# Optimization experiments

Hardware: AMD Instinct MI355X
Metric: run time of the kernel (lower is better)

Reference implementation:

```python
import jax, jax.numpy as jnp
import numpy as np


def setup_inputs() -> dict:
    key = jax.random.key(0)
    k_x, k_q, k_k, k_v = jax.random.split(key, 4)
    B, S, E, D = 4, 2048, 1024, 1024
    scale = 1.0 / np.sqrt(E)
    return {
        "x": jax.random.normal(k_x, (B, S, E), dtype=jnp.float32),
        # nn.Linear weight matrices, shape [out_dim, in_dim]; y = x @ W.T
        "w_q": jax.random.normal(k_q, (D, E), dtype=jnp.float32) * scale,
        "w_k": jax.random.normal(k_k, (D, E), dtype=jnp.float32) * scale,
        "w_v": jax.random.normal(k_v, (D, E), dtype=jnp.float32) * scale,
    }


def reference(x, w_q, w_k, w_v):
    # x: [B, S, E]; w_*: [D, E] (torch nn.Linear convention)
    B, S, E = x.shape
    q = jnp.einsum("bse,de->bsd", x, w_q)  # [B, S, D]
    k = jnp.einsum("bse,de->bsd", x, w_k)
    v = jnp.einsum("bse,de->bsd", x, w_v)
    D = q.shape[-1]
    # raw scores, then causal mask (strictly upper triangle -> -inf), then
    # scale by 1/sqrt(D) inside softmax exactly as the original does.
    scores = jnp.einsum("bsd,btd->bst", q, k)  # [B, S, S]
    causal = jnp.tril(jnp.ones((S, S), dtype=bool))  # True = keep
    scores = jnp.where(causal[None], scores, -jnp.inf)
    attn = jax.nn.softmax(scores / jnp.sqrt(jnp.asarray(D, x.dtype)), axis=-1)
    # dropout p=0.0 -> identity
    return jnp.einsum("bst,btd->bsd", attn, v)  # [B, S, D]
```

## Files before the change

kernel.cpp:

```cpp
#include <hip/hip_runtime.h>
#include <hip/hip_bf16.h>


typedef unsigned short u16;
typedef __attribute__((ext_vector_type(4))) u16   u16x4;
typedef __attribute__((ext_vector_type(8))) u16   u16x8;
typedef __attribute__((ext_vector_type(8))) short short8;
typedef __attribute__((ext_vector_type(4))) float f32x4;
typedef __attribute__((ext_vector_type(4))) int   i32x4;

__device__ inline u16 f2b(float v) {
    __hip_bfloat16 b = __float2bfloat16(v);
    return *reinterpret_cast<u16*>(&b);
}
__device__ inline float b2f(u16 v) {
    unsigned int u = ((unsigned int)v) << 16;
    return *reinterpret_cast<float*>(&u);
}

template <typename T> __device__ inline void store_elem(T* p, float v);
template <> __device__ inline void store_elem<float>(float* p, float v) { *p = v; }
template <> __device__ inline void store_elem<u16>(u16* p, float v)     { *p = f2b(v); }

__device__ inline void gload_lds16(const u16* g, u16* l) {
    __builtin_amdgcn_global_load_lds(
        (const __attribute__((address_space(1))) void*)g,
        (__attribute__((address_space(3))) void*)l, 16, 0, 0);
}

__global__ __launch_bounds__(256) void cast_all_kernel(
    const float* __restrict__ x,  const float* __restrict__ wq,
    const float* __restrict__ wk, const float* __restrict__ wv,
    u16* __restrict__ dst) {
    int q = blockIdx.x * 256 + threadIdx.x;
    const float* src;
    int sidx;
    if (q < 2097152) { src = x; sidx = q * 4; }
    else {
        int qq = q - 2097152;
        int w  = qq >> 18;
        sidx   = (qq & 262143) * 4;
        src    = (w == 0) ? wq : (w == 1) ? wk : wv;
    }
    float4 v = *(const float4*)(src + sidx);
    u16x4 o;
    o.x = f2b(v.x); o.y = f2b(v.y); o.z = f2b(v.z); o.w = f2b(v.w);
    *(u16x4*)(dst + q * 4) = o;
}

__global__ __launch_bounds__(512) void gemm_qkv256(
    const u16* __restrict__ xb, const u16* __restrict__ wb,
    u16* __restrict__ qk, u16* __restrict__ vt)
{
    __shared__ __align__(16) u16 lds[2][2][16384];

    const int tid  = threadIdx.x;
    const int lane = tid & 63;
    const int wave = tid >> 6;
    const int quad = lane >> 4;
    const int r16  = lane & 15;
    const int wm   = wave >> 2;
    const int wn   = wave & 3;

    int flat = blockIdx.x;
    int swz  = (flat & 7) * 48 + (flat >> 3);
    int bx   = swz % 12;
    int m0   = (swz / 12) * 256;
    const bool isV = (bx >= 8);
    const int  n0  = (isV ? bx - 8 : bx) * 256;
    const u16* __restrict__ Ab = xb;
    const u16* __restrict__ Bb = wb + (isV ? 2048 * 1024 : 0);

    int gA[2][2], gB[2][2], lA[2][2], lB[2][2];
    {
        const int cswz = ((lane & 3) * 8) ^ (((lane >> 5) & 1) << 4);
        const int rsub = lane >> 2;
#pragma unroll
        for (int u = 0; u < 2; ++u)
#pragma unroll
            for (int j = 0; j < 2; ++j) {
                int s   = j * 8 + wave;
                int sh  = s >> 1, cg = s & 1;
                int rgA = (sh & 3) + (sh >> 2) * 8 + u * 4;
                int rgB = sh + u * 8;
                int cl  = cg * 32 + cswz;
                gA[u][j] = (m0 + rgA * 16 + rsub) * 1024 + cl;
                gB[u][j] = (n0 + rgB * 16 + rsub) * 1024 + cl;
                lA[u][j] = (rgA * 2 + cg) * 512 + lane * 8;
                lB[u][j] = (rgB * 2 + cg) * 512 + lane * 8;
            }
    }

#define STAGE_A(BUF, U, KK) do { \
        gload_lds16(Ab + gA[U][0] + (KK), &lds[BUF][0][lA[U][0]]); \
        gload_lds16(Ab + gA[U][1] + (KK), &lds[BUF][0][lA[U][1]]); } while (0)
#define STAGE_B(BUF, U, KK) do { \
        gload_lds16(Bb + gB[U][0] + (KK), &lds[BUF][1][lB[U][0]]); \
        gload_lds16(Bb + gB[U][1] + (KK), &lds[BUF][1][lB[U][1]]); } while (0)

    const int cswr = (quad * 8) ^ ((r16 >> 3) << 4);
    const int rdA0 = wm * 16 * 512 + r16 * 32 + cswr;
    const int rdB0 = wn * 8  * 512 + r16 * 32 + cswr;

    f32x4 acc[8][4] = {};

    STAGE_B(0, 0, 0);  STAGE_B(0, 1, 0);  STAGE_A(0, 0, 0);  STAGE_A(0, 1, 0);
    STAGE_B(1, 0, 64); STAGE_B(1, 1, 64); STAGE_A(1, 0, 64); STAGE_A(1, 1, 64);
    asm volatile("s_waitcnt vmcnt(8)" ::: "memory");
    __builtin_amdgcn_s_barrier();

    for (int t = 0; t < 16; ++t) {
        const int  buf = t & 1;
        const int  kk2 = t * 64 + 128;
        const bool pf  = (t < 14);
        const u16* Al  = lds[buf][0];
        const u16* Bl  = lds[buf][1];
        short8 bfr[4][2], a01[2][2], a23[2][2], a45[2][2], a67[2][2];

#pragma unroll
        for (int nf = 0; nf < 4; ++nf)
#pragma unroll
            for (int ks = 0; ks < 2; ++ks)
                bfr[nf][ks] = *(const short8*)&Bl[rdB0 + (nf * 2 + ks) * 512];
#pragma unroll
        for (int mf = 0; mf < 2; ++mf)
#pragma unroll
            for (int ks = 0; ks < 2; ++ks)
                a01[mf][ks] = *(const short8*)&Al[rdA0 + (mf * 2 + ks) * 512];
        __builtin_amdgcn_s_barrier();
        __builtin_amdgcn_s_setprio(1);
#pragma unroll
        for (int mf = 0; mf < 2; ++mf)
#pragma unroll
            for (int nf = 0; nf < 4; ++nf)
#pragma unroll
                for (int ks = 0; ks < 2; ++ks)
                    acc[mf][nf] = __builtin_amdgcn_mfma_f32_16x16x32_bf16(
                        a01[mf][ks], bfr[nf][ks], acc[mf][nf], 0, 0, 0);
        __builtin_amdgcn_s_setprio(0);
        __builtin_amdgcn_s_barrier();

#pragma unroll
        for (int mf = 0; mf < 2; ++mf)
#pragma unroll
            for (int ks = 0; ks < 2; ++ks)
                a23[mf][ks] = *(const short8*)&Al[rdA0 + ((mf + 2) * 2 + ks) * 512];
        if (pf) STAGE_B(buf, 0, kk2);
        __builtin_amdgcn_s_barrier();
        __builtin_amdgcn_s_setprio(1);
#pragma unroll
        for (int mf = 0; mf < 2; ++mf)
#pragma unroll
            for (int nf = 0; nf < 4; ++nf)
#pragma unroll
                for (int ks = 0; ks < 2; ++ks)
                    acc[mf + 2][nf] = __builtin_amdgcn_mfma_f32_16x16x32_bf16(
                        a23[mf][ks], bfr[nf][ks], acc[mf + 2][nf], 0, 0, 0);
        __builtin_amdgcn_s_setprio(0);
        __builtin_amdgcn_s_barrier();

#pragma unroll
        for (int mf = 0; mf < 2; ++mf)
#pragma unroll
            for (int ks = 0; ks < 2; ++ks) {
                a45[mf][ks] = *(const short8*)&Al[rdA0 + ((mf + 4) * 2 + ks) * 512];
                a67[mf][ks] = *(const short8*)&Al[rdA0 + ((mf + 6) * 2 + ks) * 512];
            }
        if (pf) STAGE_B(buf, 1, kk2);
        __builtin_amdgcn_s_barrier();
        __builtin_amdgcn_s_setprio(1);
#pragma unroll
        for (int mf = 0; mf < 2; ++mf)
#pragma unroll
            for (int nf = 0; nf < 4; ++nf)
#pragma unroll
                for (int ks = 0; ks < 2; ++ks)
                    acc[mf + 4][nf] = __builtin_amdgcn_mfma_f32_16x16x32_bf16(
                        a45[mf][ks], bfr[nf][ks], acc[mf + 4][nf], 0, 0, 0);
        __builtin_amdgcn_s_setprio(0);
        asm volatile("s_waitcnt lgkmcnt(0)" ::: "memory");
        __builtin_amdgcn_s_barrier();

        if (pf) { STAGE_A(buf, 0, kk2); STAGE_A(buf, 1, kk2); }
        __builtin_amdgcn_s_barrier();
        __builtin_amdgcn_s_setprio(1);
#pragma unroll
        for (int mf = 0; mf < 2; ++mf)
#pragma unroll
            for (int nf = 0; nf < 4; ++nf)
#pragma unroll
                for (int ks = 0; ks < 2; ++ks)
                    acc[mf + 6][nf] = __builtin_amdgcn_mfma_f32_16x16x32_bf16(
                        a67[mf][ks], bfr[nf][ks], acc[mf + 6][nf], 0, 0, 0);
        __builtin_amdgcn_s_setprio(0);
        if (pf) asm volatile("s_waitcnt vmcnt(8)" ::: "memory");
        else    asm volatile("s_waitcnt vmcnt(0)" ::: "memory");
        __builtin_amdgcn_s_barrier();
    }
#undef STAGE_A
#undef STAGE_B

    if (!isV) {
#pragma unroll
        for (int mf = 0; mf < 8; ++mf) {
            int m = m0 + wm * 128 + mf * 16 + quad * 4;
#pragma unroll
            for (int nf = 0; nf < 4; ++nf) {
                int n = n0 + wn * 64 + nf * 16 + r16;
#pragma unroll
                for (int r = 0; r < 4; ++r)
                    qk[(m + r) * 2048 + n] = f2b(acc[mf][nf][r]);
            }
        }
    } else {
#pragma unroll
        for (int mf = 0; mf < 8; ++mf) {
            int mbase = m0 + wm * 128 + mf * 16 + quad * 4;
            int b = mbase >> 11;
            int s = mbase & 2047;
#pragma unroll
            for (int nf = 0; nf < 4; ++nf) {
                int d = n0 + wn * 64 + nf * 16 + r16;
                u16x4 o;
#pragma unroll
                for (int r = 0; r < 4; ++r) o[r] = f2b(acc[mf][nf][r]);
                *(u16x4*)(vt + (((b << 10) + d) * 2048 + s)) = o;
            }
        }
    }
}

#define MT 128
#define NT 128
#define BKH 32
#define HSZ (MT * BKH)

template <int TRANS, typename OutT>
__device__ __forceinline__ void gemm_core(
    u16* __restrict__ As, u16* __restrict__ Bs,
    const u16* __restrict__ Ab, int lda,
    const u16* __restrict__ Bb, int ldb,
    OutT* __restrict__ Cb, int ldc,
    int m0, int n0, int kbeg, int kend)
{
    const int tid  = threadIdx.x;
    const int lane = tid & 63;
    const int wave = tid >> 6;
    const int quad = lane >> 4;
    const int r16  = lane & 15;
    const int mw   = (wave >> 1) * 64;
    const int nw   = (wave & 1) * 64;

    const int c0 = tid, c1 = tid + 256;
    const int r0 = c0 >> 2, k0 = (c0 & 3) * 8;
    const int r1 = c1 >> 2, k1 = (c1 & 3) * 8;
    const int oa0 = (m0 + r0) * lda + k0;
    const int oa1 = (m0 + r1) * lda + k1;
    const int ob0 = (n0 + r0) * ldb + k0;
    const int ob1 = (n0 + r1) * ldb + k1;

    f32x4 acc[4][4] = {};

    for (int kk = kbeg; kk < kend; kk += 2 * BKH) {
        __syncthreads();
        gload_lds16(Ab + (kk + oa0),        &As[c0 * 8]);
        gload_lds16(Ab + (kk + oa1),        &As[c1 * 8]);
        gload_lds16(Ab + (kk + BKH + oa0),  &As[HSZ + c0 * 8]);
        gload_lds16(Ab + (kk + BKH + oa1),  &As[HSZ + c1 * 8]);
        gload_lds16(Bb + (kk + ob0),        &Bs[c0 * 8]);
        gload_lds16(Bb + (kk + ob1),        &Bs[c1 * 8]);
        gload_lds16(Bb + (kk + BKH + ob0),  &Bs[HSZ + c0 * 8]);
        gload_lds16(Bb + (kk + BKH + ob1),  &Bs[HSZ + c1 * 8]);
        __syncthreads();

#pragma unroll
        for (int h = 0; h < 2; h++) {
            short8 af[4], bf[4];
#pragma unroll
            for (int i = 0; i < 4; i++)
                af[i] = *(const short8*)&As[h * HSZ + (mw + i * 16 + r16) * BKH + quad * 8];
#pragma unroll
            for (int j = 0; j < 4; j++)
                bf[j] = *(const short8*)&Bs[h * HSZ + (nw + j * 16 + r16) * BKH + quad * 8];
#pragma unroll
            for (int i = 0; i < 4; i++)
#pragma unroll
                for (int j = 0; j < 4; j++)
                    acc[i][j] = __builtin_amdgcn_mfma_f32_16x16x32_bf16(af[i], bf[j], acc[i][j], 0, 0, 0);
        }
    }

    if (TRANS == 0) {
#pragma unroll
        for (int i = 0; i < 4; i++)
#pragma unroll
            for (int j = 0; j < 4; j++)
#pragma unroll
                for (int r = 0; r < 4; r++) {
                    int m = m0 + mw + i * 16 + quad * 4 + r;
                    int n = n0 + nw + j * 16 + r16;
                    store_elem(&Cb[(long long)m * ldc + n], acc[i][j][r]);
                }
    } else {
#pragma unroll
        for (int i = 0; i < 4; i++)
#pragma unroll
            for (int j = 0; j < 4; j++) {
                int mbase = m0 + mw + i * 16 + quad * 4;
                int d     = n0 + nw + j * 16 + r16;
                int b     = mbase >> 11;
                int s     = mbase & 2047;
                u16x4 o;
#pragma unroll
                for (int r = 0; r < 4; r++) o[r] = f2b(acc[i][j][r]);
                *(u16x4*)((u16*)Cb + (((b << 10) + d) * 2048 + s)) = o;
            }
    }
}

__global__ __launch_bounds__(256, 4) void gemm_scores(
    const u16* __restrict__ qk, u16* __restrict__ sc) {
    __shared__ __align__(16) u16 As[2 * HSZ];
    __shared__ __align__(16) u16 Bs[2 * HSZ];
    int t = blockIdx.x;
    float ff = sqrtf(8.0f * t + 1.0f);
    int m = (int)((ff - 1.0f) * 0.5f);
    while ((m + 1) * (m + 2) / 2 <= t) m++;
    while (m * (m + 1) / 2 > t) m--;
    int m0 = m * MT;
    int n0 = (t - m * (m + 1) / 2) * NT;
    const u16* Ab = qk + (long long)blockIdx.z * 2048 * 2048;
    const u16* Bb = Ab + 1024;
    u16* Cb = sc + (long long)blockIdx.z * 2048 * 2048;
    gemm_core<0, u16>(As, Bs, Ab, 2048, Bb, 2048, Cb, 2048, m0, n0, 0, 1024);
}

__global__ __launch_bounds__(256, 4) void gemm_pv(
    const u16* __restrict__ P, const u16* __restrict__ vt,
    float* __restrict__ out, float* __restrict__ part)
{
    __shared__ __align__(16) u16 As[2 * HSZ];
    __shared__ __align__(16) u16 Bs[2 * HSZ];
    const int bid = blockIdx.x;
    int m, chunk, n;
    if (bid < 80) {
        int q = bid >> 3; n = bid & 7;
        if (q < 9) { m = 7 + q; chunk = 0; } else { m = 15; chunk = 1; }
    } else {
        int r = bid - 80; int s = 7 - (r >> 4); int t = r & 15;
        n = t & 7;
        if (t < 8) { m = s - 1; chunk = 0; } else { m = s + 7; chunk = 1; }
    }
    const int m0 = m * MT, n0 = n * NT;
    const int kbeg = chunk ? 1024 : 0;
    const int kend = chunk ? (m0 + MT) : min(1024, m0 + MT);
    const int b = blockIdx.z;

    const u16* Ab = P  + (long long)b * 2048 * 2048;
    const u16* Bb = vt + (long long)b * 1024 * 2048;
    float* Cb = (chunk == 0)
        ? out  + (long long)b * 2097152
        : part + (long long)b * 1048576 - 1024LL * 1024;
    gemm_core<0, float>(As, Bs, Ab, 2048, Bb, 2048, Cb, 1024, m0, n0, kbeg, kend);
}

__global__ __launch_bounds__(256) void pv_combine(float* __restrict__ out,
                                                  const float* __restrict__ part) {
    long long idx = ((long long)blockIdx.x * 256 + threadIdx.x) * 8;
    long long bb = idx >> 20;
    long long j  = idx & 1048575;
    float* o = out + bb * 2097152 + 1048576 + j;
    const float* p = part + bb * 1048576 + j;
    float4 o0 = *(float4*)o, o1 = *(float4*)(o + 4);
    float4 p0 = *(const float4*)p, p1 = *(const float4*)(p + 4);
    o0.x += p0.x; o0.y += p0.y; o0.z += p0.z; o0.w += p0.w;
    o1.x += p1.x; o1.y += p1.y; o1.z += p1.z; o1.w += p1.w;
    *(float4*)o = o0; *(float4*)(o + 4) = o1;
}

__global__ __launch_bounds__(256) void softmax_kernel(const u16* __restrict__ sc,
                                                      u16* __restrict__ P) {
    const int S = 2048;
    int row = blockIdx.x;
    int i   = row & (S - 1);
    int n   = i + 1;
    int kendr = (i & ~127) + 128;
    const u16* srow = sc + (long long)row * S;
    u16*       prow = P  + (long long)row * S;

    int j0 = threadIdx.x * 8;
    u16x8 raw = {};
    if (j0 <= i) raw = *(const u16x8*)(srow + j0);
    float v[8];
#pragma unroll
    for (int e = 0; e < 8; e++) v[e] = (j0 + e < n) ? b2f(raw[e]) : -1e30f;

    __shared__ float red[8];
    float lmax = v[0];
#pragma unroll
    for (int e = 1; e < 8; e++) lmax = fmaxf(lmax, v[e]);
    for (int o = 32; o > 0; o >>= 1) lmax = fmaxf(lmax, __shfl_xor(lmax, o, 64));
    int wid = threadIdx.x >> 6;
    if ((threadIdx.x & 63) == 0) red[wid] = lmax;
    __syncthreads();
    float Mx = fmaxf(fmaxf(red[0], red[1]), fmaxf(red[2], red[3]));

    const float C = 0.045112384f;
    float ev[8];
    float lsum = 0.f;
#pragma unroll
    for (int e = 0; e < 8; e++) {
        ev[e] = (j0 + e < n) ? exp2f((v[e] - Mx) * C) : 0.f;
        lsum += ev[e];
    }
    for (int o = 32; o > 0; o >>= 1) lsum += __shfl_xor(lsum, o, 64);
    if ((threadIdx.x & 63) == 0) red[4 + wid] = lsum;
    __syncthreads();
    float inv = 1.0f / (red[4] + red[5] + red[6] + red[7]);

    if (j0 < kendr) {
        u16x8 o8;
#pragma unroll
        for (int e = 0; e < 8; e++) o8[e] = f2b(ev[e] * inv);
        *(u16x8*)(prow + j0) = o8;
    }
}

extern "C" void kernel_launch(void* const* d_in, const int* in_sizes, int n_in,
                              void* d_out, int out_size, void* d_ws, size_t ws_size,
                              hipStream_t stream) {
    const float* x  = (const float*)d_in[0];
    const float* wq = (const float*)d_in[1];
    const float* wk = (const float*)d_in[2];
    const float* wv = (const float*)d_in[3];
    float* out = (float*)d_out;

    char* ws = (char*)d_ws;
    u16*   xb   = (u16*)(ws);
    u16*   wb   = (u16*)(ws + 16777216LL);
    u16*   qk   = (u16*)(ws + 23068672LL);
    u16*   sc   = (u16*)(ws + 56623104LL);
    u16*   P    = (u16*)(ws + 90177536LL);
    u16*   vt   = (u16*)(ws + 123731968LL);
    float* part = (float*)(ws + 140509184LL);

    cast_all_kernel<<<11264, 256, 0, stream>>>(x, wq, wk, wv, xb);

    gemm_qkv256<<<384, 512, 0, stream>>>(xb, wb, qk, vt);

    gemm_scores<<<dim3(136, 1, 4), 256, 0, stream>>>(qk, sc);

    softmax_kernel<<<8192, 256, 0, stream>>>(sc, P);

    gemm_pv<<<dim3(192, 1, 4), 256, 0, stream>>>(P, vt, out, part);
    pv_combine<<<2048, 256, 0, stream>>>(out, part);
}
```

Measured before the change: 256.4 us.

## Move V projection into causal scores kernel and pair softmax rows per block

The V projection is taken out of the large QKV GEMM and computed by extra blocks appended to the triangular scores GEMM launch. Those extra blocks fill the load imbalance of the causal tiles, and the QK GEMM becomes a smaller launch. Softmax now handles a long row and a short row in each block, which evens out per-block work and halves the block count. The trade-off is that V now uses the smaller 128-tile GEMM core instead of the tuned 256-tile kernel, which may be less efficient for that part.

```diff
diff --git a/kernel.cpp b/kernel.cpp
--- a/kernel.cpp
+++ b/kernel.cpp
@@ -48,9 +48,9 @@
     *(u16x4*)(dst + q * 4) = o;
 }
 
-__global__ __launch_bounds__(512) void gemm_qkv256(
+__global__ __launch_bounds__(512) void gemm_qk256(
     const u16* __restrict__ xb, const u16* __restrict__ wb,
-    u16* __restrict__ qk, u16* __restrict__ vt)
+    u16* __restrict__ qk)
 {
     __shared__ __align__(16) u16 lds[2][2][16384];
 
@@ -63,13 +63,11 @@
     const int wn   = wave & 3;
 
     int flat = blockIdx.x;
-    int swz  = (flat & 7) * 48 + (flat >> 3);
-    int bx   = swz % 12;
-    int m0   = (swz / 12) * 256;
-    const bool isV = (bx >= 8);
-    const int  n0  = (isV ? bx - 8 : bx) * 256;
+    int swz  = (flat & 7) * 32 + (flat >> 3);
+    int m0   = (swz >> 3) * 256;
+    const int n0 = (swz & 7) * 256;
     const u16* __restrict__ Ab = xb;
-    const u16* __restrict__ Bb = wb + (isV ? 2048 * 1024 : 0);
+    const u16* __restrict__ Bb = wb;
 
     int gA[2][2], gB[2][2], lA[2][2], lB[2][2];
     {
@@ -200,32 +198,15 @@
 #undef STAGE_A
 #undef STAGE_B
 
-    if (!isV) {
-#pragma unroll
-        for (int mf = 0; mf < 8; ++mf) {
-            int m = m0 + wm * 128 + mf * 16 + quad * 4;
-#pragma unroll
-            for (int nf = 0; nf < 4; ++nf) {
-                int n = n0 + wn * 64 + nf * 16 + r16;
-#pragma unroll
-                for (int r = 0; r < 4; ++r)
-                    qk[(m + r) * 2048 + n] = f2b(acc[mf][nf][r]);
-            }
-        }
-    } else {
-#pragma unroll
-        for (int mf = 0; mf < 8; ++mf) {
-            int mbase = m0 + wm * 128 + mf * 16 + quad * 4;
-            int b = mbase >> 11;
-            int s = mbase & 2047;
-#pragma unroll
-            for (int nf = 0; nf < 4; ++nf) {
-                int d = n0 + wn * 64 + nf * 16 + r16;
-                u16x4 o;
-#pragma unroll
-                for (int r = 0; r < 4; ++r) o[r] = f2b(acc[mf][nf][r]);
-                *(u16x4*)(vt + (((b << 10) + d) * 2048 + s)) = o;
-            }
+#pragma unroll
+    for (int mf = 0; mf < 8; ++mf) {
+        int m = m0 + wm * 128 + mf * 16 + quad * 4;
+#pragma unroll
+        for (int nf = 0; nf < 4; ++nf) {
+            int n = n0 + wn * 64 + nf * 16 + r16;
+#pragma unroll
+            for (int r = 0; r < 4; ++r)
+                qk[(m + r) * 2048 + n] = f2b(acc[mf][nf][r]);
         }
     }
 }
@@ -318,21 +299,33 @@
     }
 }
 
-__global__ __launch_bounds__(256, 4) void gemm_scores(
-    const u16* __restrict__ qk, u16* __restrict__ sc) {
+__global__ __launch_bounds__(256, 4) void gemm_sv(
+    const u16* __restrict__ qk, u16* __restrict__ sc,
+    const u16* __restrict__ xb, const u16* __restrict__ wb,
+    u16* __restrict__ vt) {
     __shared__ __align__(16) u16 As[2 * HSZ];
     __shared__ __align__(16) u16 Bs[2 * HSZ];
-    int t = blockIdx.x;
-    float ff = sqrtf(8.0f * t + 1.0f);
-    int m = (int)((ff - 1.0f) * 0.5f);
-    while ((m + 1) * (m + 2) / 2 <= t) m++;
-    while (m * (m + 1) / 2 > t) m--;
-    int m0 = m * MT;
-    int n0 = (t - m * (m + 1) / 2) * NT;
-    const u16* Ab = qk + (long long)blockIdx.z * 2048 * 2048;
-    const u16* Bb = Ab + 1024;
-    u16* Cb = sc + (long long)blockIdx.z * 2048 * 2048;
-    gemm_core<0, u16>(As, Bs, Ab, 2048, Bb, 2048, Cb, 2048, m0, n0, 0, 1024);
+    int bid = blockIdx.x;
+    if (bid < 544) {
+        int z = bid / 136;
+        int t = bid - z * 136;
+        float ff = sqrtf(8.0f * t + 1.0f);
+        int m = (int)((ff - 1.0f) * 0.5f);
+        while ((m + 1) * (m + 2) / 2 <= t) m++;
+        while (m * (m + 1) / 2 > t) m--;
+        int m0 = m * MT;
+        int n0 = (t - m * (m + 1) / 2) * NT;
+        const u16* Ab = qk + (long long)z * 2048 * 2048;
+        const u16* Bb = Ab + 1024;
+        u16* Cb = sc + (long long)z * 2048 * 2048;
+        gemm_core<0, u16>(As, Bs, Ab, 2048, Bb, 2048, Cb, 2048, m0, n0, 0, 1024);
+    } else {
+        int vb = bid - 544;
+        int bx = vb & 7;
+        int m0 = (vb >> 3) * MT;
+        gemm_core<1, u16>(As, Bs, xb, 1024, wb + 2048 * 1024, 1024, vt, 2048,
+                          m0, bx * 128, 0, 1024);
+    }
 }
 
 __global__ __launch_bounds__(256, 4) void gemm_pv(
@@ -378,10 +371,10 @@
     *(float4*)o = o0; *(float4*)(o + 4) = o1;
 }
 
-__global__ __launch_bounds__(256) void softmax_kernel(const u16* __restrict__ sc,
-                                                      u16* __restrict__ P) {
+__device__ __forceinline__ void softmax_row(const u16* __restrict__ sc,
+                                            u16* __restrict__ P, int row,
+                                            float* __restrict__ red) {
     const int S = 2048;
-    int row = blockIdx.x;
     int i   = row & (S - 1);
     int n   = i + 1;
     int kendr = (i & ~127) + 128;
@@ -395,7 +388,6 @@
 #pragma unroll
     for (int e = 0; e < 8; e++) v[e] = (j0 + e < n) ? b2f(raw[e]) : -1e30f;
 
-    __shared__ float red[8];
     float lmax = v[0];
 #pragma unroll
     for (int e = 1; e < 8; e++) lmax = fmaxf(lmax, v[e]);
@@ -424,6 +416,15 @@
         for (int e = 0; e < 8; e++) o8[e] = f2b(ev[e] * inv);
         *(u16x8*)(prow + j0) = o8;
     }
+}
+
+__global__ __launch_bounds__(256) void softmax_kernel(const u16* __restrict__ sc,
+                                                      u16* __restrict__ P) {
+    __shared__ float red[8];
+    int i = blockIdx.x;
+    int z = blockIdx.z;
+    softmax_row(sc, P, z * 2048 + (2047 - i), red);
+    softmax_row(sc, P, z * 2048 + i, red);
 }
 
 extern "C" void kernel_launch(void* const* d_in, const int* in_sizes, int n_in,
@@ -446,11 +447,11 @@
 
     cast_all_kernel<<<11264, 256, 0, stream>>>(x, wq, wk, wv, xb);
 
-    gemm_qkv256<<<384, 512, 0, stream>>>(xb, wb, qk, vt);
-
-    gemm_scores<<<dim3(136, 1, 4), 256, 0, stream>>>(qk, sc);
-
-    softmax_kernel<<<8192, 256, 0, stream>>>(sc, P);
+    gemm_qk256<<<256, 512, 0, stream>>>(xb, wb, qk);
+
+    gemm_sv<<<1056, 256, 0, stream>>>(qk, sc, xb, wb, vt);
+
+    softmax_kernel<<<dim3(1024, 1, 4), 256, 0, stream>>>(sc, P);
 
     gemm_pv<<<dim3(192, 1, 4), 256, 0, stream>>>(P, vt, out, part);
     pv_combine<<<2048, 256, 0, stream>>>(out, part);
```

Result: faster. 247.9 us (-3.3%).
